# Performance work log

Measured on AMD Instinct MI355X. Metric: run time of the kernel, lower is better.

## Reference

```python
import jax, jax.numpy as jnp
import numpy as np

DIM = 1024
RATIO = 4
B, N = 4, 4096
EPS = 1e-5


def setup_inputs() -> dict:
    key = jax.random.key(0)
    ks = jax.random.split(key, 9)
    s = 0.02
    d, dr = DIM, DIM * RATIO
    return {
        "x": jax.random.normal(ks[0], (B, N, d), dtype=jnp.float32),
        "ln_g": jnp.ones((d,), dtype=jnp.float32),
        "ln_b": jnp.zeros((d,), dtype=jnp.float32),
        "Wq": jax.random.normal(ks[1], (d, d), dtype=jnp.float32) * s,
        "bq": jnp.zeros((d,), dtype=jnp.float32),
        "Wk": jax.random.normal(ks[2], (dr, d), dtype=jnp.float32) * s,
        "bk": jnp.zeros((d,), dtype=jnp.float32),
        "Wv": jax.random.normal(ks[3], (dr, d), dtype=jnp.float32) * s,
        "bv": jnp.zeros((d,), dtype=jnp.float32),
        "Wo": jax.random.normal(ks[4], (d, d), dtype=jnp.float32) * s,
        "bo": jnp.zeros((d,), dtype=jnp.float32),
    }


def reference(x, ln_g, ln_b, Wq, bq, Wk, bk, Wv, bv, Wo, bo):
    b, n, d = x.shape
    scale = jnp.sqrt(jnp.asarray(d, dtype=x.dtype))
    # LayerNorm over last dim
    mu = jnp.mean(x, axis=-1, keepdims=True)
    var = jnp.mean(jnp.square(x - mu), axis=-1, keepdims=True)
    xn = (x - mu) * jax.lax.rsqrt(var + EPS) * ln_g + ln_b
    # Q: (b, n, d)
    q = xn @ Wq + bq
    # fold ratio tokens together: (b, n/ratio, d*ratio)
    xr = xn.reshape(b, n // RATIO, d * RATIO)
    k = xr @ Wk + bk            # (b, m, d), m = n/ratio
    v = xr @ Wv + bv            # (b, m, d)
    scores = jnp.einsum("bnd,bmd->bnm", q, k) / scale
    attn = jax.nn.softmax(scores, axis=-1)
    out = jnp.einsum("bnm,bmd->bnd", attn, v)
    return out @ Wo + bo
```

## Files before the change

### kernel.cpp

```cpp
#include <hip/hip_runtime.h>
#include <hip/hip_bf16.h>
#include <stdint.h>

typedef __bf16 bf16x8 __attribute__((ext_vector_type(8)));
typedef float f32x4 __attribute__((ext_vector_type(4)));
typedef __hip_bfloat16 bf16;

#define D_MODEL 1024
#define BATCH 4
#define NSEQ 4096
#define NTOK (BATCH * NSEQ)
#define MTOK (BATCH * (NSEQ / 4))

__device__ __forceinline__ void async_copy16(const void* g, void* l) {
  __builtin_amdgcn_global_load_lds(
      (const __attribute__((address_space(1))) void*)g,
      (__attribute__((address_space(3))) void*)l, 16, 0, 0);
}

__device__ __forceinline__ float to_f32(float v) { return v; }
__device__ __forceinline__ float to_f32(bf16 v) { return __bfloat162float(v); }

__global__ __launch_bounds__(256) void ln_kernel(
    const float* __restrict__ x, const float* __restrict__ g,
    const float* __restrict__ b, bf16* __restrict__ xn) {
  const size_t row = blockIdx.x;
  const float4* xr = (const float4*)(x + row * D_MODEL);
  const int tid = threadIdx.x;
  float4 v = xr[tid];
  float s = v.x + v.y + v.z + v.w;
  float sq = v.x * v.x + v.y * v.y + v.z * v.z + v.w * v.w;
#pragma unroll
  for (int o = 1; o < 64; o <<= 1) {
    s += __shfl_xor(s, o);
    sq += __shfl_xor(sq, o);
  }
  __shared__ float rs[4], rq[4];
  if ((tid & 63) == 0) { rs[tid >> 6] = s; rq[tid >> 6] = sq; }
  __syncthreads();
  s = rs[0] + rs[1] + rs[2] + rs[3];
  sq = rq[0] + rq[1] + rq[2] + rq[3];
  const float mu = s * (1.f / D_MODEL);
  const float var = sq * (1.f / D_MODEL) - mu * mu;
  const float rstd = rsqrtf(var + 1e-5f);
  float4 gv = ((const float4*)g)[tid];
  float4 bv = ((const float4*)b)[tid];
  union { ushort4 u; bf16 h[4]; } pk;
  pk.h[0] = __float2bfloat16((v.x - mu) * rstd * gv.x + bv.x);
  pk.h[1] = __float2bfloat16((v.y - mu) * rstd * gv.y + bv.y);
  pk.h[2] = __float2bfloat16((v.z - mu) * rstd * gv.z + bv.z);
  pk.h[3] = __float2bfloat16((v.w - mu) * rstd * gv.w + bv.w);
  ((ushort4*)(xn + row * D_MODEL))[tid] = pk.u;
}

template <typename T>
__global__ __launch_bounds__(256) void transpose_to_bf16(
    const T* __restrict__ in, bf16* __restrict__ out, int ldin, int ldout,
    size_t inStride, size_t outStride) {
  __shared__ bf16 tile[32][33];
  const int tx = threadIdx.x;
  const int ty = threadIdx.y;
  const int c0 = blockIdx.x * 32;
  const int r0 = blockIdx.y * 32;
  const T* ip = in + (size_t)blockIdx.z * inStride;
  bf16* op = out + (size_t)blockIdx.z * outStride;
#pragma unroll
  for (int i = 0; i < 4; i++) {
    const int r = r0 + ty + i * 8;
    tile[ty + i * 8][tx] = __float2bfloat16(to_f32(ip[(size_t)r * ldin + c0 + tx]));
  }
  __syncthreads();
#pragma unroll
  for (int i = 0; i < 4; i++) {
    const int oc = c0 + ty + i * 8;
    op[(size_t)oc * ldout + r0 + tx] = tile[tx][ty + i * 8];
  }
}

__global__ __launch_bounds__(256) void pack2(const float* __restrict__ a,
                                             const float* __restrict__ b,
                                             float* __restrict__ o) {
  const int i = blockIdx.x * 256 + threadIdx.x;
  o[i] = (i < 1024) ? a[i] : b[i - 1024];
}

__global__ __launch_bounds__(256) void softmax_kernel(
    const float* __restrict__ S, bf16* __restrict__ P) {
  const size_t row = blockIdx.x;
  const float4* sp = (const float4*)(S + row * 1024);
  const int tid = threadIdx.x;
  float4 v = sp[tid];
  float mx = fmaxf(fmaxf(v.x, v.y), fmaxf(v.z, v.w));
#pragma unroll
  for (int o = 1; o < 64; o <<= 1) mx = fmaxf(mx, __shfl_xor(mx, o));
  __shared__ float red[4];
  __shared__ float red2[4];
  if ((tid & 63) == 0) red[tid >> 6] = mx;
  __syncthreads();
  mx = fmaxf(fmaxf(red[0], red[1]), fmaxf(red[2], red[3]));
  const float e0 = __expf(v.x - mx), e1 = __expf(v.y - mx);
  const float e2 = __expf(v.z - mx), e3 = __expf(v.w - mx);
  float s = e0 + e1 + e2 + e3;
#pragma unroll
  for (int o = 1; o < 64; o <<= 1) s += __shfl_xor(s, o);
  if ((tid & 63) == 0) red2[tid >> 6] = s;
  __syncthreads();
  s = red2[0] + red2[1] + red2[2] + red2[3];
  const float inv = 1.f / s;
  union { ushort4 u; bf16 h[4]; } pk;
  pk.h[0] = __float2bfloat16(e0 * inv);
  pk.h[1] = __float2bfloat16(e1 * inv);
  pk.h[2] = __float2bfloat16(e2 * inv);
  pk.h[3] = __float2bfloat16(e3 * inv);
  ((ushort4*)(P + row * 1024))[tid] = pk.u;
}

template <typename CT, bool HAS_BIAS>
__global__ __launch_bounds__(512, 2) void gemm8p(
    const bf16* __restrict__ A, const bf16* __restrict__ Bt,
    CT* __restrict__ C, const float* __restrict__ bias, float scale,
    int K, int lda, int ldb, int ldc,
    size_t aStride, size_t bStride, size_t cStride) {
  __shared__ __align__(128) char lds[131072];
  const int tid = threadIdx.x;
  const int lane = tid & 63;
  const int wid = tid >> 6;
  const int wr = wid >> 2;
  const int wc = wid & 3;
  const int bn0 = blockIdx.x * 256;
  const int bm0 = blockIdx.y * 256;
  A += (size_t)blockIdx.z * aStride;
  Bt += (size_t)blockIdx.z * bStride;
  C += (size_t)blockIdx.z * cStride;

  const bf16* pa[2];
  const bf16* pb[2];
  int lo[2];
#pragma unroll
  for (int j = 0; j < 2; j++) {
    const int o = tid * 16 + j * 8192;
    const int L = o ^ (((o >> 9) & 1) << 5);
    const int r = L >> 7;
    const int c = (L & 127) >> 1;
    pa[j] = A + (size_t)(bm0 + r) * lda + c;
    pb[j] = Bt + (size_t)(bn0 + r) * ldb + c;
    lo[j] = o;
  }

  const int arow = wr * 128 + (lane & 15);
  const int brow = wc * 64 + (lane & 15);
  const int aRd = (arow * 128 + (lane >> 4) * 16) ^ (((arow >> 2) & 1) << 5);
  const int bRd = (brow * 128 + (lane >> 4) * 16) ^ (((brow >> 2) & 1) << 5);

  bf16x8 Af[2][4][2];
  bf16x8 Bf[2][2];
  f32x4 acc[8][4];
#pragma unroll
  for (int m = 0; m < 8; m++)
#pragma unroll
    for (int n = 0; n < 4; n++) acc[m][n] = (f32x4){0.f, 0.f, 0.f, 0.f};

#define STAGE_A(b, h, kt) { const size_t go = (size_t)((h) * 128) * lda + (size_t)(kt) * 64; \
  _Pragma("unroll") for (int j = 0; j < 2; j++) \
    async_copy16(pa[j] + go, lds + (b) * 65536 + (h) * 16384 + lo[j]); }
#define STAGE_B(b, h, kt) { const size_t go = (size_t)((h) * 128) * ldb + (size_t)(kt) * 64; \
  _Pragma("unroll") for (int j = 0; j < 2; j++) \
    async_copy16(pb[j] + go, lds + (b) * 65536 + 32768 + (h) * 16384 + lo[j]); }
#define READ_A(b) _Pragma("unroll") for (int mh = 0; mh < 2; mh++) \
  _Pragma("unroll") for (int m2 = 0; m2 < 4; m2++) \
  _Pragma("unroll") for (int kk = 0; kk < 2; kk++) \
    Af[mh][m2][kk] = *(const bf16x8*)(lds + (b) * 65536 + (aRd + (mh * 4 + m2) * 2048 + kk * 64));
#define READ_B(b, nh) _Pragma("unroll") for (int n2 = 0; n2 < 2; n2++) \
  _Pragma("unroll") for (int kk = 0; kk < 2; kk++) \
    Bf[n2][kk] = *(const bf16x8*)(lds + (b) * 65536 + 32768 + (bRd + ((nh) * 2 + n2) * 2048 + kk * 64));
#define MFMA_Q(MH, NH) { __builtin_amdgcn_s_setprio(1); \
  _Pragma("unroll") for (int m2 = 0; m2 < 4; m2++) \
  _Pragma("unroll") for (int n2 = 0; n2 < 2; n2++) \
  _Pragma("unroll") for (int kk = 0; kk < 2; kk++) \
    acc[(MH) * 4 + m2][(NH) * 2 + n2] = __builtin_amdgcn_mfma_f32_16x16x32_bf16( \
        Af[MH][m2][kk], Bf[n2][kk], acc[(MH) * 4 + m2][(NH) * 2 + n2], 0, 0, 0); \
  __builtin_amdgcn_s_setprio(0); }
#define BARR() { __builtin_amdgcn_sched_barrier(0); __builtin_amdgcn_s_barrier(); __builtin_amdgcn_sched_barrier(0); }
#define LGKM0() { asm volatile("s_waitcnt lgkmcnt(0)" ::: "memory"); __builtin_amdgcn_sched_barrier(0); }
#define VMC(n) { asm volatile("s_waitcnt vmcnt(" #n ")" ::: "memory"); __builtin_amdgcn_sched_barrier(0); }

  STAGE_A(0, 0, 0) STAGE_A(0, 1, 0) STAGE_B(0, 0, 0) STAGE_B(0, 1, 0)
  STAGE_A(1, 0, 1) STAGE_A(1, 1, 1) STAGE_B(1, 0, 1)
  VMC(6)
  BARR()

  const int NIT = K >> 7;
  for (int it = 0; it < NIT - 1; ++it) {
    const int kt = it * 2;
    READ_A(0) READ_B(0, 0)
    STAGE_B(1, 1, kt + 1)
    BARR()
    MFMA_Q(0, 0)
    LGKM0()
    BARR()
    STAGE_A(0, 0, kt + 2)
    BARR()
    MFMA_Q(1, 0)
    BARR()
    READ_B(0, 1)
    STAGE_A(0, 1, kt + 2)
    BARR()
    MFMA_Q(0, 1)
    BARR()
    STAGE_B(0, 0, kt + 2)
    VMC(6)
    BARR()
    MFMA_Q(1, 1)
    BARR()
    READ_A(1) READ_B(1, 0)
    STAGE_B(0, 1, kt + 2)
    BARR()
    MFMA_Q(0, 0)
    LGKM0()
    BARR()
    STAGE_A(1, 0, kt + 3)
    BARR()
    MFMA_Q(1, 0)
    BARR()
    READ_B(1, 1)
    STAGE_A(1, 1, kt + 3)
    BARR()
    MFMA_Q(0, 1)
    BARR()
    STAGE_B(1, 0, kt + 3)
    VMC(6)
    BARR()
    MFMA_Q(1, 1)
    BARR()
  }
  {
    const int kt = (NIT - 1) * 2;
    READ_A(0) READ_B(0, 0)
    STAGE_B(1, 1, kt + 1)
    BARR()
    MFMA_Q(0, 0)
    LGKM0()
    BARR()
    MFMA_Q(1, 0)
    READ_B(0, 1)
    MFMA_Q(0, 1)
    MFMA_Q(1, 1)
    VMC(0)
    BARR()
    READ_A(1) READ_B(1, 0)
    MFMA_Q(0, 0)
    MFMA_Q(1, 0)
    READ_B(1, 1)
    MFMA_Q(0, 1)
    MFMA_Q(1, 1)
  }
#undef STAGE_A
#undef STAGE_B
#undef READ_A
#undef READ_B
#undef MFMA_Q
#undef BARR
#undef LGKM0
#undef VMC

  const int cl = lane & 15;
  const int rg = lane >> 4;
#pragma unroll
  for (int m = 0; m < 8; m++) {
#pragma unroll
    for (int n = 0; n < 4; n++) {
      const int col = bn0 + wc * 64 + n * 16 + cl;
      const float bv = HAS_BIAS ? bias[col] : 0.f;
#pragma unroll
      for (int j = 0; j < 4; j++) {
        const int row = bm0 + wr * 128 + m * 16 + rg * 4 + j;
        const float v = acc[m][n][j] * scale + bv;
        if constexpr (sizeof(CT) == 2)
          C[(size_t)row * ldc + col] = __float2bfloat16(v);
        else
          C[(size_t)row * ldc + col] = v;
      }
    }
  }
}

extern "C" void kernel_launch(void* const* d_in, const int* in_sizes, int n_in,
                              void* d_out, int out_size, void* d_ws, size_t ws_size,
                              hipStream_t stream) {
  const float* x = (const float*)d_in[0];
  const float* ln_g = (const float*)d_in[1];
  const float* ln_b = (const float*)d_in[2];
  const float* Wq = (const float*)d_in[3];
  const float* bq = (const float*)d_in[4];
  const float* Wk = (const float*)d_in[5];
  const float* bk = (const float*)d_in[6];
  const float* Wv = (const float*)d_in[7];
  const float* bv = (const float*)d_in[8];
  const float* Wo = (const float*)d_in[9];
  const float* bo = (const float*)d_in[10];
  float* out = (float*)d_out;

  char* w = (char*)d_ws;
  auto alloc = [&](size_t bytes) {
    char* p = w;
    w += (bytes + 255) & ~(size_t)255;
    return p;
  };
  bf16* xn    = (bf16*)alloc((size_t)NTOK * D_MODEL * 2);
  bf16* WqT   = (bf16*)alloc((size_t)D_MODEL * D_MODEL * 2);
  bf16* WkvT  = (bf16*)alloc((size_t)2 * D_MODEL * 4 * D_MODEL * 2);
  bf16* WoT   = (bf16*)alloc((size_t)D_MODEL * D_MODEL * 2);
  float* bkv  = (float*)alloc((size_t)2048 * 4);
  bf16* q     = (bf16*)alloc((size_t)NTOK * D_MODEL * 2);
  bf16* kv    = (bf16*)alloc((size_t)MTOK * 2048 * 2);
  bf16* vT    = (bf16*)alloc((size_t)MTOK * D_MODEL * 2);
  float* sc   = (float*)alloc((size_t)NTOK * 1024 * 4);
  bf16* attn  = (bf16*)alloc((size_t)NTOK * 1024 * 2);
  bf16* aout  = q;

  ln_kernel<<<NTOK, 256, 0, stream>>>(x, ln_g, ln_b, xn);

  transpose_to_bf16<float><<<dim3(32, 32, 1), dim3(32, 8), 0, stream>>>(Wq, WqT, 1024, 1024, 0, 0);
  transpose_to_bf16<float><<<dim3(32, 128, 1), dim3(32, 8), 0, stream>>>(Wk, WkvT, 1024, 4096, 0, 0);
  transpose_to_bf16<float><<<dim3(32, 128, 1), dim3(32, 8), 0, stream>>>(
      Wv, WkvT + (size_t)1024 * 4096, 1024, 4096, 0, 0);
  transpose_to_bf16<float><<<dim3(32, 32, 1), dim3(32, 8), 0, stream>>>(Wo, WoT, 1024, 1024, 0, 0);
  pack2<<<8, 256, 0, stream>>>(bk, bv, bkv);

  gemm8p<bf16, true><<<dim3(4, 64, 1), 512, 0, stream>>>(
      xn, WqT, q, bq, 1.f, 1024, 1024, 1024, 1024, 0, 0, 0);

  gemm8p<bf16, true><<<dim3(8, 16, 1), 512, 0, stream>>>(
      xn, WkvT, kv, bkv, 1.f, 4096, 4096, 4096, 2048, 0, 0, 0);

  transpose_to_bf16<bf16><<<dim3(32, 32, BATCH), dim3(32, 8), 0, stream>>>(
      kv + 1024, vT, 2048, 1024, (size_t)1024 * 2048, (size_t)1024 * 1024);

  gemm8p<float, false><<<dim3(4, 16, 4), 512, 0, stream>>>(
      q, kv, sc, nullptr, 0.03125f, 1024, 1024, 2048, 1024,
      (size_t)4096 * 1024, (size_t)1024 * 2048, (size_t)4096 * 1024);

  softmax_kernel<<<NTOK, 256, 0, stream>>>(sc, attn);

  gemm8p<bf16, false><<<dim3(4, 16, 4), 512, 0, stream>>>(
      attn, vT, aout, nullptr, 1.f, 1024, 1024, 1024, 1024,
      (size_t)4096 * 1024, (size_t)1024 * 1024, (size_t)4096 * 1024);

  gemm8p<float, true><<<dim3(4, 64, 1), 512, 0, stream>>>(
      aout, WoT, out, bo, 1.f, 1024, 1024, 1024, 1024, 0, 0, 0);
}
```

Before: 473.7 us.

## Template GEMM on M-tile size, remap blocks across XCDs, restructure pipeline

```diff
diff --git a/kernel.cpp b/kernel.cpp
--- a/kernel.cpp
+++ b/kernel.cpp
@@ -115,165 +115,198 @@
   ((ushort4*)(P + row * 1024))[tid] = pk.u;
 }
 
-template <typename CT, bool HAS_BIAS>
-__global__ __launch_bounds__(512, 2) void gemm8p(
+template <typename CT, bool HAS_BIAS, int MFR>
+__global__ __launch_bounds__(512, 1) void gemm8p(
     const bf16* __restrict__ A, const bf16* __restrict__ Bt,
     CT* __restrict__ C, const float* __restrict__ bias, float scale,
     int K, int lda, int ldb, int ldc,
     size_t aStride, size_t bStride, size_t cStride) {
-  __shared__ __align__(128) char lds[131072];
+  constexpr int BM = MFR * 32;
+  constexpr int AHALF = MFR * 2048;
+  constexpr int ABUF = MFR * 4096;
+  constexpr int BUFS = ABUF + 32768;
+  constexpr int AL = MFR / 4;
+  __shared__ __align__(128) char lds[2 * BUFS];
+
   const int tid = threadIdx.x;
   const int lane = tid & 63;
   const int wid = tid >> 6;
   const int wr = wid >> 2;
   const int wc = wid & 3;
-  const int bn0 = blockIdx.x * 256;
-  const int bm0 = blockIdx.y * 256;
-  A += (size_t)blockIdx.z * aStride;
-  Bt += (size_t)blockIdx.z * bStride;
-  C += (size_t)blockIdx.z * cStride;
-
-  const bf16* pa[2];
+
+  const int nx = gridDim.x, ny = gridDim.y;
+  const int shx = __popc(nx - 1), shy = __popc(ny - 1);
+  const int lxy = nx * ny;
+  int lin = blockIdx.x + nx * blockIdx.y + lxy * blockIdx.z;
+  const int nwg = lxy * gridDim.z;
+  lin = (lin & 7) * (nwg >> 3) + (lin >> 3);
+  const int bx = lin & (nx - 1);
+  const int by = (lin >> shx) & (ny - 1);
+  const int bz = lin >> (shx + shy);
+
+  const int bn0 = bx * 256;
+  const int bm0 = by * BM;
+  A += (size_t)bz * aStride;
+  Bt += (size_t)bz * bStride;
+  C += (size_t)bz * cStride;
+
+  const bf16* pa[AL];
+  int loA[AL];
   const bf16* pb[2];
-  int lo[2];
+  int loB[2];
+#pragma unroll
+  for (int j = 0; j < AL; j++) {
+    const int o = tid * 16 + j * 8192;
+    const int L = o ^ (((o >> 9) & 1) << 5);
+    pa[j] = A + (size_t)(bm0 + (L >> 7)) * lda + ((L & 127) >> 1);
+    loA[j] = o;
+  }
 #pragma unroll
   for (int j = 0; j < 2; j++) {
     const int o = tid * 16 + j * 8192;
     const int L = o ^ (((o >> 9) & 1) << 5);
-    const int r = L >> 7;
-    const int c = (L & 127) >> 1;
-    pa[j] = A + (size_t)(bm0 + r) * lda + c;
-    pb[j] = Bt + (size_t)(bn0 + r) * ldb + c;
-    lo[j] = o;
-  }
-
-  const int arow = wr * 128 + (lane & 15);
+    pb[j] = Bt + (size_t)(bn0 + (L >> 7)) * ldb + ((L & 127) >> 1);
+    loB[j] = o;
+  }
+
+  const int arow = wr * (MFR * 16) + (lane & 15);
   const int brow = wc * 64 + (lane & 15);
   const int aRd = (arow * 128 + (lane >> 4) * 16) ^ (((arow >> 2) & 1) << 5);
   const int bRd = (brow * 128 + (lane >> 4) * 16) ^ (((brow >> 2) & 1) << 5);
 
-  bf16x8 Af[2][4][2];
-  bf16x8 Bf[2][2];
-  f32x4 acc[8][4];
-#pragma unroll
-  for (int m = 0; m < 8; m++)
+  bf16x8 Ah[MFR / 2][2];
+  bf16x8 B0f[2][2], B1f[2][2];
+  f32x4 acc[MFR][4];
+#pragma unroll
+  for (int m = 0; m < MFR; m++)
 #pragma unroll
     for (int n = 0; n < 4; n++) acc[m][n] = (f32x4){0.f, 0.f, 0.f, 0.f};
 
-#define STAGE_A(b, h, kt) { const size_t go = (size_t)((h) * 128) * lda + (size_t)(kt) * 64; \
-  _Pragma("unroll") for (int j = 0; j < 2; j++) \
-    async_copy16(pa[j] + go, lds + (b) * 65536 + (h) * 16384 + lo[j]); }
+#define STAGE_A(b, h, kt) { const size_t go = (size_t)((h) * (BM / 2)) * lda + (size_t)(kt) * 64; \
+  _Pragma("unroll") for (int j = 0; j < AL; j++) \
+    async_copy16(pa[j] + go, lds + (b) * BUFS + (h) * AHALF + loA[j]); }
 #define STAGE_B(b, h, kt) { const size_t go = (size_t)((h) * 128) * ldb + (size_t)(kt) * 64; \
   _Pragma("unroll") for (int j = 0; j < 2; j++) \
-    async_copy16(pb[j] + go, lds + (b) * 65536 + 32768 + (h) * 16384 + lo[j]); }
-#define READ_A(b) _Pragma("unroll") for (int mh = 0; mh < 2; mh++) \
-  _Pragma("unroll") for (int m2 = 0; m2 < 4; m2++) \
+    async_copy16(pb[j] + go, lds + (b) * BUFS + ABUF + (h) * 16384 + loB[j]); }
+#define READ_A(b, h) _Pragma("unroll") for (int m2 = 0; m2 < MFR / 2; m2++) \
   _Pragma("unroll") for (int kk = 0; kk < 2; kk++) \
-    Af[mh][m2][kk] = *(const bf16x8*)(lds + (b) * 65536 + (aRd + (mh * 4 + m2) * 2048 + kk * 64));
-#define READ_B(b, nh) _Pragma("unroll") for (int n2 = 0; n2 < 2; n2++) \
+    Ah[m2][kk] = *(const bf16x8*)(lds + (b) * BUFS + (aRd + ((h) * (MFR / 2) + m2) * 2048 + kk * 64));
+#define READ_B0(b) _Pragma("unroll") for (int n2 = 0; n2 < 2; n2++) \
   _Pragma("unroll") for (int kk = 0; kk < 2; kk++) \
-    Bf[n2][kk] = *(const bf16x8*)(lds + (b) * 65536 + 32768 + (bRd + ((nh) * 2 + n2) * 2048 + kk * 64));
-#define MFMA_Q(MH, NH) { __builtin_amdgcn_s_setprio(1); \
-  _Pragma("unroll") for (int m2 = 0; m2 < 4; m2++) \
+    B0f[n2][kk] = *(const bf16x8*)(lds + (b) * BUFS + ABUF + (bRd + n2 * 2048 + kk * 64));
+#define READ_B1(b) _Pragma("unroll") for (int n2 = 0; n2 < 2; n2++) \
+  _Pragma("unroll") for (int kk = 0; kk < 2; kk++) \
+    B1f[n2][kk] = *(const bf16x8*)(lds + (b) * BUFS + ABUF + (bRd + (2 + n2) * 2048 + kk * 64));
+#define MFMA_Q(MH, NH, BF) { __builtin_amdgcn_s_setprio(1); \
+  _Pragma("unroll") for (int m2 = 0; m2 < MFR / 2; m2++) \
   _Pragma("unroll") for (int n2 = 0; n2 < 2; n2++) \
   _Pragma("unroll") for (int kk = 0; kk < 2; kk++) \
-    acc[(MH) * 4 + m2][(NH) * 2 + n2] = __builtin_amdgcn_mfma_f32_16x16x32_bf16( \
-        Af[MH][m2][kk], Bf[n2][kk], acc[(MH) * 4 + m2][(NH) * 2 + n2], 0, 0, 0); \
+    acc[(MH) * (MFR / 2) + m2][(NH) * 2 + n2] = __builtin_amdgcn_mfma_f32_16x16x32_bf16( \
+        Ah[m2][kk], BF[n2][kk], acc[(MH) * (MFR / 2) + m2][(NH) * 2 + n2], 0, 0, 0); \
   __builtin_amdgcn_s_setprio(0); }
 #define BARR() { __builtin_amdgcn_sched_barrier(0); __builtin_amdgcn_s_barrier(); __builtin_amdgcn_sched_barrier(0); }
-#define LGKM0() { asm volatile("s_waitcnt lgkmcnt(0)" ::: "memory"); __builtin_amdgcn_sched_barrier(0); }
-#define VMC(n) { asm volatile("s_waitcnt vmcnt(" #n ")" ::: "memory"); __builtin_amdgcn_sched_barrier(0); }
+#define VMC4() { asm volatile("s_waitcnt vmcnt(4)" ::: "memory"); __builtin_amdgcn_sched_barrier(0); }
+#define VMCN() { if constexpr (AL == 2) { asm volatile("s_waitcnt vmcnt(6)" ::: "memory"); } \
+                 else { asm volatile("s_waitcnt vmcnt(4)" ::: "memory"); } \
+                 __builtin_amdgcn_sched_barrier(0); }
+#define VMC0() { asm volatile("s_waitcnt vmcnt(0)" ::: "memory"); __builtin_amdgcn_sched_barrier(0); }
 
   STAGE_A(0, 0, 0) STAGE_A(0, 1, 0) STAGE_B(0, 0, 0) STAGE_B(0, 1, 0)
   STAGE_A(1, 0, 1) STAGE_A(1, 1, 1) STAGE_B(1, 0, 1)
-  VMC(6)
+  VMCN()
   BARR()
 
   const int NIT = K >> 7;
   for (int it = 0; it < NIT - 1; ++it) {
     const int kt = it * 2;
-    READ_A(0) READ_B(0, 0)
+    READ_A(0, 0) READ_B0(0)
     STAGE_B(1, 1, kt + 1)
     BARR()
-    MFMA_Q(0, 0)
-    LGKM0()
-    BARR()
+    MFMA_Q(0, 0, B0f)
+    BARR()
+    READ_B1(0)
+    BARR()
+    MFMA_Q(0, 1, B1f)
+    BARR()
+    READ_A(0, 1)
+    STAGE_B(0, 0, kt + 2)
+    BARR()
+    MFMA_Q(1, 0, B0f)
+    BARR()
+    STAGE_B(0, 1, kt + 2)
+    VMC4()
+    BARR()
+    MFMA_Q(1, 1, B1f)
+    BARR()
+    READ_A(1, 0) READ_B0(1)
     STAGE_A(0, 0, kt + 2)
     BARR()
-    MFMA_Q(1, 0)
-    BARR()
-    READ_B(0, 1)
+    MFMA_Q(0, 0, B0f)
+    BARR()
+    READ_B1(1)
     STAGE_A(0, 1, kt + 2)
     BARR()
-    MFMA_Q(0, 1)
-    BARR()
-    STAGE_B(0, 0, kt + 2)
-    VMC(6)
-    BARR()
-    MFMA_Q(1, 1)
-    BARR()
-    READ_A(1) READ_B(1, 0)
-    STAGE_B(0, 1, kt + 2)
-    BARR()
-    MFMA_Q(0, 0)
-    LGKM0()
-    BARR()
-    STAGE_A(1, 0, kt + 3)
-    BARR()
-    MFMA_Q(1, 0)
-    BARR()
-    READ_B(1, 1)
-    STAGE_A(1, 1, kt + 3)
-    BARR()
-    MFMA_Q(0, 1)
-    BARR()
+    MFMA_Q(0, 1, B1f)
+    BARR()
+    READ_A(1, 1)
     STAGE_B(1, 0, kt + 3)
-    VMC(6)
-    BARR()
-    MFMA_Q(1, 1)
+    BARR()
+    MFMA_Q(1, 0, B0f)
+    BARR()
+    STAGE_A(1, 0, kt + 3) STAGE_A(1, 1, kt + 3)
+    VMCN()
+    BARR()
+    MFMA_Q(1, 1, B1f)
     BARR()
   }
   {
-    const int kt = (NIT - 1) * 2;
-    READ_A(0) READ_B(0, 0)
-    STAGE_B(1, 1, kt + 1)
-    BARR()
-    MFMA_Q(0, 0)
-    LGKM0()
-    BARR()
-    MFMA_Q(1, 0)
-    READ_B(0, 1)
-    MFMA_Q(0, 1)
-    MFMA_Q(1, 1)
-    VMC(0)
-    BARR()
-    READ_A(1) READ_B(1, 0)
-    MFMA_Q(0, 0)
-    MFMA_Q(1, 0)
-    READ_B(1, 1)
-    MFMA_Q(0, 1)
-    MFMA_Q(1, 1)
+    READ_A(0, 0) READ_B0(0)
+    STAGE_B(1, 1, 2 * NIT - 1)
+    BARR()
+    MFMA_Q(0, 0, B0f)
+    BARR()
+    READ_B1(0)
+    BARR()
+    MFMA_Q(0, 1, B1f)
+    BARR()
+    READ_A(0, 1)
+    BARR()
+    MFMA_Q(1, 0, B0f)
+    BARR()
+    VMC0()
+    BARR()
+    MFMA_Q(1, 1, B1f)
+    BARR()
+    READ_A(1, 0) READ_B0(1)
+    MFMA_Q(0, 0, B0f)
+    READ_B1(1)
+    MFMA_Q(0, 1, B1f)
+    READ_A(1, 1)
+    MFMA_Q(1, 0, B0f)
+    MFMA_Q(1, 1, B1f)
   }
 #undef STAGE_A
 #undef STAGE_B
 #undef READ_A
-#undef READ_B
+#undef READ_B0
+#undef READ_B1
 #undef MFMA_Q
 #undef BARR
-#undef LGKM0
-#undef VMC
+#undef VMC4
+#undef VMCN
+#undef VMC0
 
   const int cl = lane & 15;
   const int rg = lane >> 4;
 #pragma unroll
-  for (int m = 0; m < 8; m++) {
+  for (int m = 0; m < MFR; m++) {
 #pragma unroll
     for (int n = 0; n < 4; n++) {
       const int col = bn0 + wc * 64 + n * 16 + cl;
       const float bv = HAS_BIAS ? bias[col] : 0.f;
 #pragma unroll
       for (int j = 0; j < 4; j++) {
-        const int row = bm0 + wr * 128 + m * 16 + rg * 4 + j;
+        const int row = bm0 + wr * (MFR * 16) + m * 16 + rg * 4 + j;
         const float v = acc[m][n][j] * scale + bv;
         if constexpr (sizeof(CT) == 2)
           C[(size_t)row * ldc + col] = __float2bfloat16(v);
@@ -327,25 +360,25 @@
   transpose_to_bf16<float><<<dim3(32, 32, 1), dim3(32, 8), 0, stream>>>(Wo, WoT, 1024, 1024, 0, 0);
   pack2<<<8, 256, 0, stream>>>(bk, bv, bkv);
 
-  gemm8p<bf16, true><<<dim3(4, 64, 1), 512, 0, stream>>>(
+  gemm8p<bf16, true, 8><<<dim3(4, 64, 1), 512, 0, stream>>>(
       xn, WqT, q, bq, 1.f, 1024, 1024, 1024, 1024, 0, 0, 0);
 
-  gemm8p<bf16, true><<<dim3(8, 16, 1), 512, 0, stream>>>(
+  gemm8p<bf16, true, 4><<<dim3(8, 32, 1), 512, 0, stream>>>(
       xn, WkvT, kv, bkv, 1.f, 4096, 4096, 4096, 2048, 0, 0, 0);
 
   transpose_to_bf16<bf16><<<dim3(32, 32, BATCH), dim3(32, 8), 0, stream>>>(
       kv + 1024, vT, 2048, 1024, (size_t)1024 * 2048, (size_t)1024 * 1024);
 
-  gemm8p<float, false><<<dim3(4, 16, 4), 512, 0, stream>>>(
+  gemm8p<float, false, 8><<<dim3(4, 16, 4), 512, 0, stream>>>(
       q, kv, sc, nullptr, 0.03125f, 1024, 1024, 2048, 1024,
       (size_t)4096 * 1024, (size_t)1024 * 2048, (size_t)4096 * 1024);
 
   softmax_kernel<<<NTOK, 256, 0, stream>>>(sc, attn);
 
-  gemm8p<bf16, false><<<dim3(4, 16, 4), 512, 0, stream>>>(
+  gemm8p<bf16, false, 8><<<dim3(4, 16, 4), 512, 0, stream>>>(
       attn, vT, aout, nullptr, 1.f, 1024, 1024, 1024, 1024,
       (size_t)4096 * 1024, (size_t)1024 * 1024, (size_t)4096 * 1024);
 
-  gemm8p<float, true><<<dim3(4, 64, 1), 512, 0, stream>>>(
+  gemm8p<float, true, 8><<<dim3(4, 64, 1), 512, 0, stream>>>(
       aout, WoT, out, bo, 1.f, 1024, 1024, 1024, 1024, 0, 0, 0);
 }
```

After: 418.2 us. 11.7% less time.
